# Kernel optimization log

Hardware: AMD Instinct MI355X
Metric: run time of the kernel (lower is better)

## Reference

```python
import jax, jax.numpy as jnp
import numpy as np

P = 16          # patch size
NH = 12         # num heads
DH = 64         # head dim
C = 768         # embed dim
DEPTH = 12
HID = 3072      # mlp hidden = 4*C
EPS = 1e-6


def _ln(x, g, b):
    m = x.mean(-1, keepdims=True)
    v = ((x - m) ** 2).mean(-1, keepdims=True)
    return (x - m) / jnp.sqrt(v + EPS) * g + b


def _rope_tables(seq_len, dim):
    inv_freq = 1.0 / (10000.0 ** (jnp.arange(0, dim, 2, dtype=jnp.float32) / dim))
    freqs = jnp.arange(seq_len, dtype=jnp.float32)[:, None] * inv_freq[None, :]  # [S, dim/2]
    emb = jnp.concatenate([freqs, freqs], axis=-1)  # [S, dim] (concat layout, as in source)
    return jnp.cos(emb), jnp.sin(emb)


def _apply_rope(q, k, cos, sin):
    def rot(t):  # interleaved rotate-half, exactly as torch source
        t1, t2 = t[..., ::2], t[..., 1::2]
        return jnp.stack([-t2, t1], axis=-1).reshape(t.shape)
    return q * cos + rot(q) * sin, k * cos + rot(k) * sin


def setup_inputs() -> dict:
    key = jax.random.key(0)
    ks = jax.random.split(key, 16)
    w = lambda k, shp: (jax.random.normal(k, shp, dtype=jnp.float32) * 0.02)
    inp = {
        "x": jax.random.normal(ks[0], (4, 6, 320, 320), dtype=jnp.float32),
        "conv_w": w(ks[1], (C, 3, P, P)),
        "conv_b": jnp.zeros((C,), jnp.float32),
        "ln1_g": jnp.ones((DEPTH, C), jnp.float32),
        "ln1_b": jnp.zeros((DEPTH, C), jnp.float32),
        "qkv_w": w(ks[2], (DEPTH, C, 3 * C)),
        "qkv_b": jnp.zeros((DEPTH, 3 * C), jnp.float32),
        "proj_w": w(ks[3], (DEPTH, C, C)),
        "proj_b": jnp.zeros((DEPTH, C), jnp.float32),
        "ln2_g": jnp.ones((DEPTH, C), jnp.float32),
        "ln2_b": jnp.zeros((DEPTH, C), jnp.float32),
        "fc1_w": w(ks[4], (DEPTH, C, HID)),
        "fc1_b": jnp.zeros((DEPTH, HID), jnp.float32),
        "fc2_w": w(ks[5], (DEPTH, HID, C)),
        "fc2_b": jnp.zeros((DEPTH, C), jnp.float32),
        "lnf_g": jnp.ones((C,), jnp.float32),
        "lnf_b": jnp.zeros((C,), jnp.float32),
    }
    return inp


def reference(x, conv_w, conv_b, ln1_g, ln1_b, qkv_w, qkv_b, proj_w, proj_b,
              ln2_g, ln2_b, fc1_w, fc1_b, fc2_w, fc2_b, lnf_g, lnf_b):
    B = x.shape[0]

    def embed(img):  # [B,3,H,W] -> [B, (H/P)*(W/P), C]
        y = jax.lax.conv_general_dilated(
            img, conv_w, window_strides=(P, P), padding="VALID",
            dimension_numbers=("NCHW", "OIHW", "NCHW")) + conv_b[None, :, None, None]
        b, c, hg, wg = y.shape
        return y.reshape(b, c, hg * wg).transpose(0, 2, 1)

    t = jnp.concatenate([embed(x[:, :3]), embed(x[:, 3:])], axis=1)  # [B,S,C], S=2*400=800
    S = t.shape[1]
    cos, sin = _rope_tables(S, DH)
    cos, sin = cos[None, None], sin[None, None]  # [1,1,S,DH]
    scale = DH ** -0.5

    def block(h, p):
        l1g, l1b, qw, qb, pw, pb, l2g, l2b, f1w, f1b, f2w, f2b = p
        y = _ln(h, l1g, l1b)
        qkv = (y @ qw + qb).reshape(B, S, 3, NH, DH).transpose(2, 0, 3, 1, 4)
        q, k, v = qkv[0], qkv[1], qkv[2]  # [B,NH,S,DH]
        q, k = _apply_rope(q, k, cos, sin)
        a = jax.nn.softmax(jnp.einsum("bhsd,bhtd->bhst", q, k) * scale, axis=-1)
        o = jnp.einsum("bhst,bhtd->bhsd", a, v).transpose(0, 2, 1, 3).reshape(B, S, C)
        h = h + (o @ pw + pb)
        y = _ln(h, l2g, l2b)
        h = h + (jax.nn.gelu(y @ f1w + f1b, approximate=False) @ f2w + f2b)
        return h, None

    params = (ln1_g, ln1_b, qkv_w, qkv_b, proj_w, proj_b,
              ln2_g, ln2_b, fc1_w, fc1_b, fc2_w, fc2_b)
    t, _ = jax.lax.scan(block, t, params)
    return _ln(t, lnf_g, lnf_b)
```

## Files before the change

kernel.cpp:

```cpp
#include <hip/hip_runtime.h>
#include <hip/hip_bf16.h>
#include <math.h>

#define S_LEN   800
#define SP_LEN  896
#define C_DIM   768
#define NHEAD   12
#define DHEAD   64
#define HID_DIM 3072
#define BATCH   4
#define NTOK    (BATCH * S_LEN)
#define DEPTH_N 12

using bf16x8 = __attribute__((ext_vector_type(8))) short;
using bf16x4 = __attribute__((ext_vector_type(4))) short;
using f32x4  = __attribute__((ext_vector_type(4))) float;

__device__ inline short f2bf(float x) {
    unsigned u = __builtin_bit_cast(unsigned, x);
    u += 0x7fff + ((u >> 16) & 1);
    return (short)(u >> 16);
}
__device__ inline float bf2f(short x) {
    unsigned u = ((unsigned)(unsigned short)x) << 16;
    return __builtin_bit_cast(float, u);
}

typedef const __attribute__((address_space(1))) void* gas_ptr;
typedef __attribute__((address_space(3))) void* las_ptr;
__device__ inline void async_copy16(const void* g, void* l) {
    __builtin_amdgcn_global_load_lds((gas_ptr)g, (las_ptr)l, 16, 0, 0);
}

__device__ inline int xcd_remap(int bid, int nwg) {
    int x = bid & 7, q = nwg >> 3, r = nwg & 7;
    int base = (x < r) ? x * (q + 1) : r * (q + 1) + (x - r) * q;
    return base + (bid >> 3);
}

template <int K, int N>
__device__ __forceinline__ void tc_tile(const float* __restrict__ W,
                                        short* __restrict__ Wt, int t) {
    __shared__ float tile[32][33];
    int nb = t % (N / 32), kb = t / (N / 32);
    int k0 = kb * 32, n0 = nb * 32;
    int tx = threadIdx.x & 31, ty = threadIdx.x >> 5;
#pragma unroll
    for (int i = ty; i < 32; i += 8)
        tile[i][tx] = W[(size_t)(k0 + i) * N + n0 + tx];
    __syncthreads();
#pragma unroll
    for (int i = ty; i < 32; i += 8)
        Wt[(size_t)(n0 + i) * K + k0 + tx] = f2bf(tile[tx][i]);
}

__global__ __launch_bounds__(256)
void transpose_all_kernel(const float* __restrict__ qkv_w, const float* __restrict__ proj_w,
                          const float* __restrict__ fc1_w, const float* __restrict__ fc2_w,
                          short* __restrict__ wq, short* __restrict__ wp,
                          short* __restrict__ w1, short* __restrict__ w2) {
    int t = blockIdx.x;
    int l = t / 6912, u = t % 6912;
    if (u < 1728)
        tc_tile<768, 2304>(qkv_w + (size_t)l * 768 * 2304, wq + (size_t)l * 2304 * 768, u);
    else if (u < 2304)
        tc_tile<768, 768>(proj_w + (size_t)l * 768 * 768, wp + (size_t)l * 768 * 768, u - 1728);
    else if (u < 4608)
        tc_tile<768, 3072>(fc1_w + (size_t)l * 768 * 3072, w1 + (size_t)l * 3072 * 768, u - 2304);
    else
        tc_tile<3072, 768>(fc2_w + (size_t)l * 3072 * 768, w2 + (size_t)l * 768 * 3072, u - 4608);
}

__global__ void convert_bf_kernel(const float* __restrict__ a, short* __restrict__ o, int n) {
    int i = blockIdx.x * 256 + threadIdx.x;
    if (i < n) o[i] = f2bf(a[i]);
}

__global__ void im2col_kernel(const float* __restrict__ x, short* __restrict__ A) {
    int idx = blockIdx.x * 256 + threadIdx.x;
    if (idx >= NTOK * 768) return;
    int kk = idx % 768;
    int s  = (idx / 768) % S_LEN;
    int b  = idx / (768 * S_LEN);
    int c  = kk / 256;
    int i  = (kk / 16) % 16;
    int j  = kk % 16;
    int half = s / 400, ss = s % 400;
    int hg = ss / 20, wg = ss % 20;
    int ch = half * 3 + c;
    A[idx] = f2bf(x[((size_t)(b * 6 + ch) * 320 + hg * 16 + i) * 320 + wg * 16 + j]);
}

template <int BN, bool GELU, bool RES, bool OBF>
__global__ __launch_bounds__(256)
void gemm_mfma(const short* __restrict__ A, const short* __restrict__ Bt,
               const float* __restrict__ bias, const float* __restrict__ res,
               void* __restrict__ Cout, int M, int N, int K) {
    constexpr int BM = 128, BK = 64;
    constexpr int TI = (BN == 128) ? 4 : 2;
    constexpr int TJ = 4;
    constexpr int ACALLS = BM * BK / (8 * 64);
    constexpr int BCALLS = BN * BK / (8 * 64);

    __shared__ __align__(16) short As[BM * BK];
    __shared__ __align__(16) short Bs[BN * BK];

    int tid = threadIdx.x;
    int w = tid >> 6, lane = tid & 63;

    int nwg = gridDim.x * gridDim.y;
    int flat = xcd_remap(blockIdx.x + gridDim.x * blockIdx.y, nwg);
    int bx = flat % gridDim.x, by = flat / gridDim.x;
    int m0 = by * BM, n0 = bx * BN;

    int wr = (BN == 128) ? (w >> 1) * 64 : w * 32;
    int wc = (BN == 128) ? (w & 1) * 64 : 0;

    f32x4 acc[TI][TJ];
#pragma unroll
    for (int i = 0; i < TI; ++i)
#pragma unroll
        for (int j = 0; j < TJ; ++j)
            acc[i][j] = (f32x4){0.f, 0.f, 0.f, 0.f};

    int lc = lane & 15, lq = lane >> 4;

    for (int k0 = 0; k0 < K; k0 += BK) {
#pragma unroll
        for (int j = w; j < ACALLS; j += 4) {
            int c = j * 64 + lane;
            int row = c >> 3, p = c & 7, q = p ^ (row & 7);
            async_copy16(A + (size_t)(m0 + row) * K + k0 + q * 8, As + j * 512);
        }
#pragma unroll
        for (int j = w; j < BCALLS; j += 4) {
            int c = j * 64 + lane;
            int row = c >> 3, p = c & 7, q = p ^ (row & 7);
            async_copy16(Bt + (size_t)(n0 + row) * K + k0 + q * 8, Bs + j * 512);
        }
        __syncthreads();

#pragma unroll
        for (int h = 0; h < 2; ++h) {
            bf16x8 afrag[TI], bfrag[TJ];
#pragma unroll
            for (int i = 0; i < TI; ++i) {
                int row = wr + i * 16 + lc;
                afrag[i] = *(const bf16x8*)(As + row * 64 + ((((h << 2) | lq)) ^ (row & 7)) * 8);
            }
#pragma unroll
            for (int j = 0; j < TJ; ++j) {
                int col = wc + j * 16 + lc;
                bfrag[j] = *(const bf16x8*)(Bs + col * 64 + ((((h << 2) | lq)) ^ (col & 7)) * 8);
            }
#pragma unroll
            for (int i = 0; i < TI; ++i)
#pragma unroll
                for (int j = 0; j < TJ; ++j)
                    acc[i][j] = __builtin_amdgcn_mfma_f32_16x16x32_bf16(
                        afrag[i], bfrag[j], acc[i][j], 0, 0, 0);
        }
        __syncthreads();
    }

    int rbase = lq * 4;
#pragma unroll
    for (int i = 0; i < TI; ++i)
#pragma unroll
        for (int j = 0; j < TJ; ++j)
#pragma unroll
            for (int r = 0; r < 4; ++r) {
                int m = m0 + wr + i * 16 + rbase + r;
                int n = n0 + wc + j * 16 + lc;
                float v = acc[i][j][r] + bias[n];
                if (RES) v += res[(size_t)m * N + n];
                if (GELU) v = 0.5f * v * (1.0f + erff(v * 0.70710678118654752f));
                if (OBF) ((short*)Cout)[(size_t)m * N + n] = f2bf(v);
                else     ((float*)Cout)[(size_t)m * N + n] = v;
            }
}

template <bool OBF>
__global__ __launch_bounds__(256)
void ln_kernel(const float* __restrict__ x, const float* __restrict__ g,
               const float* __restrict__ bta, void* __restrict__ yv) {
    int row = blockIdx.x;
    const float* xr = x + (size_t)row * C_DIM;
    int tid = threadIdx.x;

    float v0 = xr[tid], v1 = xr[tid + 256], v2 = xr[tid + 512];
    float s  = v0 + v1 + v2;
    float sq = v0 * v0 + v1 * v1 + v2 * v2;
#pragma unroll
    for (int off = 32; off; off >>= 1) {
        s  += __shfl_down(s, off);
        sq += __shfl_down(sq, off);
    }
    __shared__ float red1[4], red2[4];
    __shared__ float mean_s, rstd_s;
    int wv = tid / 64, lane = tid % 64;
    if (lane == 0) { red1[wv] = s; red2[wv] = sq; }
    __syncthreads();
    if (tid == 0) {
        float S1 = red1[0] + red1[1] + red1[2] + red1[3];
        float S2 = red2[0] + red2[1] + red2[2] + red2[3];
        float m = S1 / (float)C_DIM;
        float var = S2 / (float)C_DIM - m * m;
        mean_s = m;
        rstd_s = rsqrtf(var + 1e-6f);
    }
    __syncthreads();
    float m = mean_s, r = rstd_s;
    float o0 = (v0 - m) * r * g[tid]       + bta[tid];
    float o1 = (v1 - m) * r * g[tid + 256] + bta[tid + 256];
    float o2 = (v2 - m) * r * g[tid + 512] + bta[tid + 512];
    if (OBF) {
        short* yr = (short*)yv + (size_t)row * C_DIM;
        yr[tid] = f2bf(o0); yr[tid + 256] = f2bf(o1); yr[tid + 512] = f2bf(o2);
    } else {
        float* yr = (float*)yv + (size_t)row * C_DIM;
        yr[tid] = o0; yr[tid + 256] = o1; yr[tid + 512] = o2;
    }
}

__global__ __launch_bounds__(256)
void rope_qkv_kernel(const short* __restrict__ qkv, short* __restrict__ qb,
                     short* __restrict__ kb, short* __restrict__ vtb) {
    int bh = blockIdx.x;
    int st = blockIdx.y;
    int b = bh / NHEAD, h = bh % NHEAD;
    int s0 = st * 64;

    __shared__ __align__(16) short vlds[64][72];

    int tid = threadIdx.x;
    int sl = tid >> 2;
    int dc = (tid & 3) * 16;
    int s = s0 + sl;

    short qo[16], ko[16];
    if (s < S_LEN) {
        const short* base = qkv + ((size_t)(b * S_LEN + s)) * (3 * C_DIM) + h * DHEAD + dc;
        short qsh[16], ksh[16], vsh[16];
        *(bf16x8*)(qsh)     = *(const bf16x8*)(base);
        *(bf16x8*)(qsh + 8) = *(const bf16x8*)(base + 8);
        *(bf16x8*)(ksh)     = *(const bf16x8*)(base + C_DIM);
        *(bf16x8*)(ksh + 8) = *(const bf16x8*)(base + C_DIM + 8);
        *(bf16x8*)(vsh)     = *(const bf16x8*)(base + 2 * C_DIM);
        *(bf16x8*)(vsh + 8) = *(const bf16x8*)(base + 2 * C_DIM + 8);
        float qv[16], kv[16];
#pragma unroll
        for (int i = 0; i < 16; ++i) { qv[i] = bf2f(qsh[i]); kv[i] = bf2f(ksh[i]); }
#pragma unroll
        for (int i = 0; i < 16; ++i) {
            int d = dc + i;
            float ang = (float)s * exp2f(-(float)(d & 31) * 0.41524101186092029f);
            float c = cosf(ang), sn = sinf(ang);
            float sign = (i & 1) ? 1.0f : -1.0f;
            qo[i] = f2bf((qv[i] * c + sign * qv[i ^ 1] * sn) * 0.18033688011112042f);
            ko[i] = f2bf(kv[i] * c + sign * kv[i ^ 1] * sn);
        }
        *(bf16x8*)&vlds[sl][dc]     = *(bf16x8*)(vsh);
        *(bf16x8*)&vlds[sl][dc + 8] = *(bf16x8*)(vsh + 8);
    } else {
#pragma unroll
        for (int i = 0; i < 16; ++i) { qo[i] = 0; ko[i] = 0; vlds[sl][dc + i] = 0; }
    }
    {
        short* qd = qb + ((size_t)bh * SP_LEN + s) * DHEAD + dc;
        short* kd = kb + ((size_t)bh * SP_LEN + s) * DHEAD + dc;
        *(bf16x8*)(qd)     = *(bf16x8*)(qo);
        *(bf16x8*)(qd + 8) = *(bf16x8*)(qo + 8);
        *(bf16x8*)(kd)     = *(bf16x8*)(ko);
        *(bf16x8*)(kd + 8) = *(bf16x8*)(ko + 8);
    }
    __syncthreads();
    {
        int dr = tid >> 2, sc = (tid & 3) * 16;
        short vo[16];
#pragma unroll
        for (int i = 0; i < 16; ++i) vo[i] = vlds[sc + i][dr];
        short* vd = vtb + ((size_t)bh * DHEAD + dr) * SP_LEN + s0 + sc;
        *(bf16x8*)(vd)     = *(bf16x8*)(vo);
        *(bf16x8*)(vd + 8) = *(bf16x8*)(vo + 8);
    }
}

__global__ __launch_bounds__(256)
void attn_mfma_kernel(const short* __restrict__ qb, const short* __restrict__ kb,
                      const short* __restrict__ vtb, short* __restrict__ o) {
    int bh = blockIdx.x;
    int qt = blockIdx.y;
    int b = bh / NHEAD, h = bh % NHEAD;
    int m0 = qt * 64;

    __shared__ __align__(16) short Qs[64 * 64];
    __shared__ __align__(16) short Ks[128 * 64];
    __shared__ __align__(16) short Vts[64 * 128];
    __shared__ __align__(16) short Ps[64 * 136];

    int tid = threadIdx.x;
    int w = tid >> 6, lane = tid & 63;
    int lc = lane & 15, lq = lane >> 4;
    int kq = lq * 8;

    const short* qbase = qb + (size_t)bh * SP_LEN * DHEAD;
    const short* kbase = kb + (size_t)bh * SP_LEN * DHEAD;
    const short* vbase = vtb + (size_t)bh * DHEAD * SP_LEN;

    f32x4 oacc[4];
#pragma unroll
    for (int t = 0; t < 4; ++t) oacc[t] = (f32x4){0.f, 0.f, 0.f, 0.f};
    float mrow = -3.0e38f;
    float lrow = 0.f;

#pragma unroll
    for (int j = w; j < 8; j += 4) {
        int c = j * 64 + lane;
        int row = c >> 3, p = c & 7, q = p ^ (row & 7);
        async_copy16(qbase + (size_t)(m0 + row) * DHEAD + q * 8, Qs + j * 512);
    }

    bf16x8 aq0, aq1;

    for (int it = 0; it < 7; ++it) {
        int kt = it * 128;
#pragma unroll
        for (int j = w; j < 16; j += 4) {
            int c = j * 64 + lane;
            int row = c >> 3, p = c & 7, q = p ^ (row & 7);
            async_copy16(kbase + (size_t)(kt + row) * DHEAD + q * 8, Ks + j * 512);
        }
#pragma unroll
        for (int j = w; j < 16; j += 4) {
            int c = j * 64 + lane;
            int d = c >> 4, p = c & 15, sq = p ^ (d & 15);
            async_copy16(vbase + (size_t)d * SP_LEN + kt + sq * 8, Vts + j * 512);
        }
        __syncthreads();

        int nt = (it < 6) ? 8 : 2;

        if (it == 0) {
            int qrow = w * 16 + lc;
            aq0 = *(const bf16x8*)(Qs + qrow * 64 + ((lq) ^ (qrow & 7)) * 8);
            aq1 = *(const bf16x8*)(Qs + qrow * 64 + ((4 | lq) ^ (qrow & 7)) * 8);
        }

        f32x4 sacc[8];
        __builtin_amdgcn_s_setprio(1);
        for (int t = 0; t < nt; ++t) {
            int kr = t * 16 + lc;
            bf16x8 bk0 = *(const bf16x8*)(Ks + kr * 64 + ((lq) ^ (kr & 7)) * 8);
            bf16x8 bk1 = *(const bf16x8*)(Ks + kr * 64 + ((4 | lq) ^ (kr & 7)) * 8);
            f32x4 z = (f32x4){0.f, 0.f, 0.f, 0.f};
            z = __builtin_amdgcn_mfma_f32_16x16x32_bf16(bk0, aq0, z, 0, 0, 0);
            z = __builtin_amdgcn_mfma_f32_16x16x32_bf16(bk1, aq1, z, 0, 0, 0);
            sacc[t] = z;
        }
        __builtin_amdgcn_s_setprio(0);

        float rmx = sacc[0][0];
#pragma unroll
        for (int t = 0; t < nt; ++t)
#pragma unroll
            for (int r = 0; r < 4; ++r) rmx = fmaxf(rmx, sacc[t][r]);
        rmx = fmaxf(rmx, __shfl_xor(rmx, 16));
        rmx = fmaxf(rmx, __shfl_xor(rmx, 32));

        float mnew = fmaxf(mrow, rmx);
        float alpha = exp2f(mrow - mnew);
        mrow = mnew;

        float rsum = 0.f;
        for (int t = 0; t < nt; ++t) {
            bf16x4 pk;
#pragma unroll
            for (int r = 0; r < 4; ++r) {
                float p = exp2f(sacc[t][r] - mrow);
                rsum += p;
                pk[r] = f2bf(p);
            }
            *(bf16x4*)(Ps + (w * 16 + lc) * 136 + t * 16 + lq * 4) = pk;
        }
        rsum += __shfl_xor(rsum, 16);
        rsum += __shfl_xor(rsum, 32);
        lrow = lrow * alpha + rsum;

#pragma unroll
        for (int r = 0; r < 4; ++r) {
            float ar = __shfl(alpha, lq * 4 + r);
#pragma unroll
            for (int t = 0; t < 4; ++t) oacc[t][r] *= ar;
        }

        int nk = (nt == 8) ? 4 : 1;
        __builtin_amdgcn_s_setprio(1);
        for (int kstep = 0; kstep < nk; ++kstep) {
            bf16x8 ap = *(const bf16x8*)(Ps + (w * 16 + lc) * 136 + kstep * 32 + kq);
#pragma unroll
            for (int t = 0; t < 4; ++t) {
                int dr = t * 16 + lc;
                bf16x8 bv = *(const bf16x8*)(Vts + dr * 128 + ((((kstep << 2) | lq)) ^ (dr & 15)) * 8);
                oacc[t] = __builtin_amdgcn_mfma_f32_16x16x32_bf16(ap, bv, oacc[t], 0, 0, 0);
            }
        }
        __builtin_amdgcn_s_setprio(0);
        __syncthreads();
    }

    float rl = 1.0f / lrow;
    float inv_l[4];
#pragma unroll
    for (int r = 0; r < 4; ++r) inv_l[r] = __shfl(rl, lq * 4 + r);
#pragma unroll
    for (int t = 0; t < 4; ++t)
#pragma unroll
        for (int r = 0; r < 4; ++r) {
            int row = w * 16 + lq * 4 + r;
            int s = m0 + row;
            if (s < S_LEN) {
                int n = t * 16 + lc;
                o[((size_t)(b * S_LEN + s)) * C_DIM + h * DHEAD + n] = f2bf(oacc[t][r] * inv_l[r]);
            }
        }
}

extern "C" void kernel_launch(void* const* d_in, const int* in_sizes, int n_in,
                              void* d_out, int out_size, void* d_ws, size_t ws_size,
                              hipStream_t stream) {
    const float* x      = (const float*)d_in[0];
    const float* conv_w = (const float*)d_in[1];
    const float* conv_b = (const float*)d_in[2];
    const float* ln1_g  = (const float*)d_in[3];
    const float* ln1_b  = (const float*)d_in[4];
    const float* qkv_w  = (const float*)d_in[5];
    const float* qkv_b  = (const float*)d_in[6];
    const float* proj_w = (const float*)d_in[7];
    const float* proj_b = (const float*)d_in[8];
    const float* ln2_g  = (const float*)d_in[9];
    const float* ln2_b  = (const float*)d_in[10];
    const float* fc1_w  = (const float*)d_in[11];
    const float* fc1_b  = (const float*)d_in[12];
    const float* fc2_w  = (const float*)d_in[13];
    const float* fc2_b  = (const float*)d_in[14];
    const float* lnf_g  = (const float*)d_in[15];
    const float* lnf_b  = (const float*)d_in[16];

    const size_t NTC = (size_t)NTOK * C_DIM;
    const size_t HSD = (size_t)BATCH * NHEAD * SP_LEN * DHEAD;
    const size_t WQ_L = (size_t)3 * C_DIM * C_DIM;
    const size_t WP_L = (size_t)C_DIM * C_DIM;
    const size_t W1_L = (size_t)C_DIM * HID_DIM;
    const size_t W2_L = (size_t)HID_DIM * C_DIM;

    float* ws = (float*)d_ws;
    float* h       = ws;
    short* qkv_bf  = (short*)(h + NTC);
    short* qb      = qkv_bf + (size_t)NTOK * 3 * C_DIM;
    short* kb      = qb + HSD;
    short* vtb     = kb + HSD;
    short* y_bf    = vtb + HSD;
    short* big_bf  = y_bf + NTC;
    short* wq_all  = big_bf + (size_t)NTOK * HID_DIM;
    short* wp_all  = wq_all + DEPTH_N * WQ_L;
    short* w1_all  = wp_all + DEPTH_N * WP_L;
    short* w2_all  = w1_all + DEPTH_N * W1_L;
    short* embed_wt = w2_all + DEPTH_N * W2_L;

    convert_bf_kernel<<<(768 * 768 + 255) / 256, 256, 0, stream>>>(conv_w, embed_wt, 768 * 768);
    transpose_all_kernel<<<DEPTH_N * 6912, 256, 0, stream>>>(
        qkv_w, proj_w, fc1_w, fc2_w, wq_all, wp_all, w1_all, w2_all);

    im2col_kernel<<<(NTOK * 768 + 255) / 256, 256, 0, stream>>>(x, big_bf);
    gemm_mfma<64, false, false, false><<<dim3(C_DIM / 64, NTOK / 128), 256, 0, stream>>>(
        big_bf, embed_wt, conv_b, nullptr, h, NTOK, C_DIM, C_DIM);

    for (int l = 0; l < DEPTH_N; ++l) {
        const float* l1g = ln1_g + (size_t)l * C_DIM;
        const float* l1b = ln1_b + (size_t)l * C_DIM;
        const float* qbs = qkv_b + (size_t)l * 3 * C_DIM;
        const float* pb  = proj_b + (size_t)l * C_DIM;
        const float* l2g = ln2_g + (size_t)l * C_DIM;
        const float* l2b = ln2_b + (size_t)l * C_DIM;
        const float* f1b = fc1_b + (size_t)l * HID_DIM;
        const float* f2b = fc2_b + (size_t)l * C_DIM;
        const short* wq = wq_all + (size_t)l * WQ_L;
        const short* wp = wp_all + (size_t)l * WP_L;
        const short* w1 = w1_all + (size_t)l * W1_L;
        const short* w2 = w2_all + (size_t)l * W2_L;

        ln_kernel<true><<<NTOK, 256, 0, stream>>>(h, l1g, l1b, y_bf);
        gemm_mfma<128, false, false, true><<<dim3(3 * C_DIM / 128, NTOK / 128), 256, 0, stream>>>(
            y_bf, wq, qbs, nullptr, qkv_bf, NTOK, 3 * C_DIM, C_DIM);

        rope_qkv_kernel<<<dim3(BATCH * NHEAD, 14), 256, 0, stream>>>(qkv_bf, qb, kb, vtb);
        attn_mfma_kernel<<<dim3(BATCH * NHEAD, 13), 256, 0, stream>>>(qb, kb, vtb, y_bf);

        gemm_mfma<64, false, true, false><<<dim3(C_DIM / 64, NTOK / 128), 256, 0, stream>>>(
            y_bf, wp, pb, h, h, NTOK, C_DIM, C_DIM);

        ln_kernel<true><<<NTOK, 256, 0, stream>>>(h, l2g, l2b, y_bf);
        gemm_mfma<128, true, false, true><<<dim3(HID_DIM / 128, NTOK / 128), 256, 0, stream>>>(
            y_bf, w1, f1b, nullptr, big_bf, NTOK, HID_DIM, C_DIM);
        gemm_mfma<64, false, true, false><<<dim3(C_DIM / 64, NTOK / 128), 256, 0, stream>>>(
            big_bf, w2, f2b, h, h, NTOK, C_DIM, HID_DIM);
    }

    ln_kernel<false><<<NTOK, 256, 0, stream>>>(h, lnf_g, lnf_b, d_out);
}
```

Measured before the change: 2.645 ms.

## Fuse RoPE and head scatter into QKV GEMM epilogue; widen weight transpose tiles

Replaces the separate rope_qkv kernel with a dedicated QKV GEMM whose epilogue adds bias, applies rotary embedding through a lane shuffle, and writes q, k and transposed v directly in head-major padded layout. This removes the intermediate qkv buffer round trip and one launch per layer. Sequence padding is now zeroed once by a separate kernel. The weight transpose also moves to 64x64 tiles with vectorized loads and stores. The fused epilogue writes scattered scalar bf16 values, and the transposed v stores are strided, so write coalescing may suffer.

```diff
diff --git a/kernel.cpp b/kernel.cpp
--- a/kernel.cpp
+++ b/kernel.cpp
@@ -39,19 +39,30 @@
 }
 
 template <int K, int N>
-__device__ __forceinline__ void tc_tile(const float* __restrict__ W,
-                                        short* __restrict__ Wt, int t) {
-    __shared__ float tile[32][33];
-    int nb = t % (N / 32), kb = t / (N / 32);
-    int k0 = kb * 32, n0 = nb * 32;
-    int tx = threadIdx.x & 31, ty = threadIdx.x >> 5;
-#pragma unroll
-    for (int i = ty; i < 32; i += 8)
-        tile[i][tx] = W[(size_t)(k0 + i) * N + n0 + tx];
+__device__ __forceinline__ void tc64(const float* __restrict__ W,
+                                     short* __restrict__ Wt, int t) {
+    __shared__ float tile[64][65];
+    int nb = t % (N / 64), kb = t / (N / 64);
+    int k0 = kb * 64, n0 = nb * 64;
+    int tid = threadIdx.x;
+    int nf = (tid & 15) * 4;
+    int kr = tid >> 4;
+#pragma unroll
+    for (int rr = 0; rr < 4; ++rr) {
+        int k = kr + 16 * rr;
+        f32x4 v = *(const f32x4*)(W + (size_t)(k0 + k) * N + n0 + nf);
+        tile[k][nf] = v[0]; tile[k][nf + 1] = v[1];
+        tile[k][nf + 2] = v[2]; tile[k][nf + 3] = v[3];
+    }
     __syncthreads();
-#pragma unroll
-    for (int i = ty; i < 32; i += 8)
-        Wt[(size_t)(n0 + i) * K + k0 + tx] = f2bf(tile[tx][i]);
+    int n = tid >> 2;
+    int kc = (tid & 3) * 16;
+    short out[16];
+#pragma unroll
+    for (int ii = 0; ii < 16; ++ii) out[ii] = f2bf(tile[kc + ii][n]);
+    short* dst = Wt + (size_t)(n0 + n) * K + k0 + kc;
+    *(bf16x8*)(dst)     = *(bf16x8*)(out);
+    *(bf16x8*)(dst + 8) = *(bf16x8*)(out + 8);
 }
 
 __global__ __launch_bounds__(256)
@@ -60,20 +71,32 @@
                           short* __restrict__ wq, short* __restrict__ wp,
                           short* __restrict__ w1, short* __restrict__ w2) {
     int t = blockIdx.x;
-    int l = t / 6912, u = t % 6912;
-    if (u < 1728)
-        tc_tile<768, 2304>(qkv_w + (size_t)l * 768 * 2304, wq + (size_t)l * 2304 * 768, u);
-    else if (u < 2304)
-        tc_tile<768, 768>(proj_w + (size_t)l * 768 * 768, wp + (size_t)l * 768 * 768, u - 1728);
-    else if (u < 4608)
-        tc_tile<768, 3072>(fc1_w + (size_t)l * 768 * 3072, w1 + (size_t)l * 3072 * 768, u - 2304);
+    int l = t / 1728, u = t % 1728;
+    if (u < 432)
+        tc64<768, 2304>(qkv_w + (size_t)l * 768 * 2304, wq + (size_t)l * 2304 * 768, u);
+    else if (u < 576)
+        tc64<768, 768>(proj_w + (size_t)l * 768 * 768, wp + (size_t)l * 768 * 768, u - 432);
+    else if (u < 1152)
+        tc64<768, 3072>(fc1_w + (size_t)l * 768 * 3072, w1 + (size_t)l * 3072 * 768, u - 576);
     else
-        tc_tile<3072, 768>(fc2_w + (size_t)l * 3072 * 768, w2 + (size_t)l * 768 * 3072, u - 4608);
+        tc64<3072, 768>(fc2_w + (size_t)l * 3072 * 768, w2 + (size_t)l * 768 * 3072, u - 1152);
 }
 
 __global__ void convert_bf_kernel(const float* __restrict__ a, short* __restrict__ o, int n) {
     int i = blockIdx.x * 256 + threadIdx.x;
     if (i < n) o[i] = f2bf(a[i]);
+}
+
+__global__ void zero_pads_kernel(short* __restrict__ qb, short* __restrict__ kb,
+                                 short* __restrict__ vtb) {
+    int i = blockIdx.x * 256 + threadIdx.x;
+    if (i >= 48 * 96 * 64) return;
+    int bh = i / (96 * 64), rem = i % (96 * 64);
+    int s = 800 + rem / 64, d = rem % 64;
+    qb[((size_t)bh * SP_LEN + s) * DHEAD + d] = 0;
+    kb[((size_t)bh * SP_LEN + s) * DHEAD + d] = 0;
+    int d2 = (i / 96) % 64, s2 = 800 + (i % 96), bh2 = i / (96 * 64);
+    vtb[((size_t)bh2 * DHEAD + d2) * SP_LEN + s2] = 0;
 }
 
 __global__ void im2col_kernel(const float* __restrict__ x, short* __restrict__ A) {
@@ -180,6 +203,105 @@
             }
 }
 
+__global__ __launch_bounds__(256)
+void gemm_qkv_rope(const short* __restrict__ A, const short* __restrict__ Bt,
+                   const float* __restrict__ bias, short* __restrict__ qb,
+                   short* __restrict__ kb, short* __restrict__ vtb,
+                   int M, int N, int K) {
+    constexpr int BM = 128, BN = 128, BK = 64;
+    constexpr int TI = 4, TJ = 4;
+
+    __shared__ __align__(16) short As[BM * BK];
+    __shared__ __align__(16) short Bs[BN * BK];
+
+    int tid = threadIdx.x;
+    int w = tid >> 6, lane = tid & 63;
+
+    int nwg = gridDim.x * gridDim.y;
+    int flat = xcd_remap(blockIdx.x + gridDim.x * blockIdx.y, nwg);
+    int bx = flat % gridDim.x, by = flat / gridDim.x;
+    int m0 = by * BM, n0 = bx * BN;
+
+    int wr = (w >> 1) * 64, wc = (w & 1) * 64;
+
+    f32x4 acc[TI][TJ];
+#pragma unroll
+    for (int i = 0; i < TI; ++i)
+#pragma unroll
+        for (int j = 0; j < TJ; ++j)
+            acc[i][j] = (f32x4){0.f, 0.f, 0.f, 0.f};
+
+    int lc = lane & 15, lq = lane >> 4;
+
+    for (int k0 = 0; k0 < K; k0 += BK) {
+#pragma unroll
+        for (int j = w; j < 16; j += 4) {
+            int c = j * 64 + lane;
+            int row = c >> 3, p = c & 7, q = p ^ (row & 7);
+            async_copy16(A + (size_t)(m0 + row) * K + k0 + q * 8, As + j * 512);
+        }
+#pragma unroll
+        for (int j = w; j < 16; j += 4) {
+            int c = j * 64 + lane;
+            int row = c >> 3, p = c & 7, q = p ^ (row & 7);
+            async_copy16(Bt + (size_t)(n0 + row) * K + k0 + q * 8, Bs + j * 512);
+        }
+        __syncthreads();
+
+#pragma unroll
+        for (int h = 0; h < 2; ++h) {
+            bf16x8 afrag[TI], bfrag[TJ];
+#pragma unroll
+            for (int i = 0; i < TI; ++i) {
+                int row = wr + i * 16 + lc;
+                afrag[i] = *(const bf16x8*)(As + row * 64 + ((((h << 2) | lq)) ^ (row & 7)) * 8);
+            }
+#pragma unroll
+            for (int j = 0; j < TJ; ++j) {
+                int col = wc + j * 16 + lc;
+                bfrag[j] = *(const bf16x8*)(Bs + col * 64 + ((((h << 2) | lq)) ^ (col & 7)) * 8);
+            }
+#pragma unroll
+            for (int i = 0; i < TI; ++i)
+#pragma unroll
+                for (int j = 0; j < TJ; ++j)
+                    acc[i][j] = __builtin_amdgcn_mfma_f32_16x16x32_bf16(
+                        afrag[i], bfrag[j], acc[i][j], 0, 0, 0);
+        }
+        __syncthreads();
+    }
+
+    int comp = n0 / 768;
+#pragma unroll
+    for (int i = 0; i < TI; ++i)
+#pragma unroll
+        for (int j = 0; j < TJ; ++j)
+#pragma unroll
+            for (int r = 0; r < 4; ++r) {
+                int m = m0 + wr + i * 16 + lq * 4 + r;
+                int n = n0 + wc + j * 16 + lc;
+                float v = acc[i][j][r] + bias[n];
+                int b = m / 800, s = m - b * 800;
+                int d = n & 63;
+                int bh = b * NHEAD + ((n >> 6) % NHEAD);
+                if (comp < 2) {
+                    float v2 = __shfl_xor(v, 1);
+                    float ang = (float)s * exp2f(-(float)(d & 31) * 0.41524101186092029f);
+                    float c = cosf(ang), sn = sinf(ang);
+                    float sign = (d & 1) ? 1.0f : -1.0f;
+                    float out = v * c + sign * v2 * sn;
+                    if (comp == 0) {
+                        out *= 0.18033688011112042f;
+                        qb[((size_t)bh * SP_LEN + s) * DHEAD + d] = f2bf(out);
+                    } else {
+                        kb[((size_t)bh * SP_LEN + s) * DHEAD + d] = f2bf(out);
+                    }
+                } else {
+                    vtb[((size_t)bh * DHEAD + d) * SP_LEN + s] = f2bf(v);
+                }
+            }
+}
+
 template <bool OBF>
 __global__ __launch_bounds__(256)
 void ln_kernel(const float* __restrict__ x, const float* __restrict__ g,
@@ -220,69 +342,6 @@
     } else {
         float* yr = (float*)yv + (size_t)row * C_DIM;
         yr[tid] = o0; yr[tid + 256] = o1; yr[tid + 512] = o2;
-    }
-}
-
-__global__ __launch_bounds__(256)
-void rope_qkv_kernel(const short* __restrict__ qkv, short* __restrict__ qb,
-                     short* __restrict__ kb, short* __restrict__ vtb) {
-    int bh = blockIdx.x;
-    int st = blockIdx.y;
-    int b = bh / NHEAD, h = bh % NHEAD;
-    int s0 = st * 64;
-
-    __shared__ __align__(16) short vlds[64][72];
-
-    int tid = threadIdx.x;
-    int sl = tid >> 2;
-    int dc = (tid & 3) * 16;
-    int s = s0 + sl;
-
-    short qo[16], ko[16];
-    if (s < S_LEN) {
-        const short* base = qkv + ((size_t)(b * S_LEN + s)) * (3 * C_DIM) + h * DHEAD + dc;
-        short qsh[16], ksh[16], vsh[16];
-        *(bf16x8*)(qsh)     = *(const bf16x8*)(base);
-        *(bf16x8*)(qsh + 8) = *(const bf16x8*)(base + 8);
-        *(bf16x8*)(ksh)     = *(const bf16x8*)(base + C_DIM);
-        *(bf16x8*)(ksh + 8) = *(const bf16x8*)(base + C_DIM + 8);
-        *(bf16x8*)(vsh)     = *(const bf16x8*)(base + 2 * C_DIM);
-        *(bf16x8*)(vsh + 8) = *(const bf16x8*)(base + 2 * C_DIM + 8);
-        float qv[16], kv[16];
-#pragma unroll
-        for (int i = 0; i < 16; ++i) { qv[i] = bf2f(qsh[i]); kv[i] = bf2f(ksh[i]); }
-#pragma unroll
-        for (int i = 0; i < 16; ++i) {
-            int d = dc + i;
-            float ang = (float)s * exp2f(-(float)(d & 31) * 0.41524101186092029f);
-            float c = cosf(ang), sn = sinf(ang);
-            float sign = (i & 1) ? 1.0f : -1.0f;
-            qo[i] = f2bf((qv[i] * c + sign * qv[i ^ 1] * sn) * 0.18033688011112042f);
-            ko[i] = f2bf(kv[i] * c + sign * kv[i ^ 1] * sn);
-        }
-        *(bf16x8*)&vlds[sl][dc]     = *(bf16x8*)(vsh);
-        *(bf16x8*)&vlds[sl][dc + 8] = *(bf16x8*)(vsh + 8);
-    } else {
-#pragma unroll
-        for (int i = 0; i < 16; ++i) { qo[i] = 0; ko[i] = 0; vlds[sl][dc + i] = 0; }
-    }
-    {
-        short* qd = qb + ((size_t)bh * SP_LEN + s) * DHEAD + dc;
-        short* kd = kb + ((size_t)bh * SP_LEN + s) * DHEAD + dc;
-        *(bf16x8*)(qd)     = *(bf16x8*)(qo);
-        *(bf16x8*)(qd + 8) = *(bf16x8*)(qo + 8);
-        *(bf16x8*)(kd)     = *(bf16x8*)(ko);
-        *(bf16x8*)(kd + 8) = *(bf16x8*)(ko + 8);
-    }
-    __syncthreads();
-    {
-        int dr = tid >> 2, sc = (tid & 3) * 16;
-        short vo[16];
-#pragma unroll
-        for (int i = 0; i < 16; ++i) vo[i] = vlds[sc + i][dr];
-        short* vd = vtb + ((size_t)bh * DHEAD + dr) * SP_LEN + s0 + sc;
-        *(bf16x8*)(vd)     = *(bf16x8*)(vo);
-        *(bf16x8*)(vd + 8) = *(bf16x8*)(vo + 8);
     }
 }
 
@@ -456,8 +515,7 @@
 
     float* ws = (float*)d_ws;
     float* h       = ws;
-    short* qkv_bf  = (short*)(h + NTC);
-    short* qb      = qkv_bf + (size_t)NTOK * 3 * C_DIM;
+    short* qb      = (short*)(h + NTC);
     short* kb      = qb + HSD;
     short* vtb     = kb + HSD;
     short* y_bf    = vtb + HSD;
@@ -469,8 +527,9 @@
     short* embed_wt = w2_all + DEPTH_N * W2_L;
 
     convert_bf_kernel<<<(768 * 768 + 255) / 256, 256, 0, stream>>>(conv_w, embed_wt, 768 * 768);
-    transpose_all_kernel<<<DEPTH_N * 6912, 256, 0, stream>>>(
+    transpose_all_kernel<<<DEPTH_N * 1728, 256, 0, stream>>>(
         qkv_w, proj_w, fc1_w, fc2_w, wq_all, wp_all, w1_all, w2_all);
+    zero_pads_kernel<<<(48 * 96 * 64 + 255) / 256, 256, 0, stream>>>(qb, kb, vtb);
 
     im2col_kernel<<<(NTOK * 768 + 255) / 256, 256, 0, stream>>>(x, big_bf);
     gemm_mfma<64, false, false, false><<<dim3(C_DIM / 64, NTOK / 128), 256, 0, stream>>>(
@@ -491,10 +550,9 @@
         const short* w2 = w2_all + (size_t)l * W2_L;
 
         ln_kernel<true><<<NTOK, 256, 0, stream>>>(h, l1g, l1b, y_bf);
-        gemm_mfma<128, false, false, true><<<dim3(3 * C_DIM / 128, NTOK / 128), 256, 0, stream>>>(
-            y_bf, wq, qbs, nullptr, qkv_bf, NTOK, 3 * C_DIM, C_DIM);
-
-        rope_qkv_kernel<<<dim3(BATCH * NHEAD, 14), 256, 0, stream>>>(qkv_bf, qb, kb, vtb);
+        gemm_qkv_rope<<<dim3(3 * C_DIM / 128, NTOK / 128), 256, 0, stream>>>(
+            y_bf, wq, qbs, qb, kb, vtb, NTOK, 3 * C_DIM, C_DIM);
+
         attn_mfma_kernel<<<dim3(BATCH * NHEAD, 13), 256, 0, stream>>>(qb, kb, vtb, y_bf);
 
         gemm_mfma<64, false, true, false><<<dim3(C_DIM / 64, NTOK / 128), 256, 0, stream>>>(
```

Result: slower. 3.535 ms (+33.6%).
